# Kernel tuning notes

Measured on AMD Instinct MI355X. Metric: run time of the kernel, lower is better.

## Reference

```python
import jax, jax.numpy as jnp
import numpy as np

TOPK = 60            # candidates kept by top-k
THRESHOLD = 0.15     # score threshold (post-sigmoid)
NMS_THRESHOLD = 0.05 # IoU overlap for suppression/matching
NMS_TOPK = 20        # max kept detections per image
CROP_SIZE = (96, 96, 96)
AVG_TOPN = 7         # max matched boxes averaged per kept box


def setup_inputs() -> dict:
    key = jax.random.key(0)
    k1, k2, k3 = jax.random.split(key, 3)
    B, D, H, W = 256, 24, 24, 24
    Cls = jax.random.normal(k1, (B, 1, D, H, W), dtype=jnp.float32)
    # sizes in [1,7) voxels so 3D boxes at stride-4 anchor spacing overlap
    Shape = jax.random.uniform(k2, (B, 3, D, H, W), dtype=jnp.float32) * 6.0 + 1.0
    Offset = jax.random.normal(k3, (B, 3, D, H, W), dtype=jnp.float32)
    return {"Cls": Cls, "Shape": Shape, "Offset": Offset}


def _decode(Cls, Shape, Offset):
    # make_anchors + bbox_decode: centers = (anchor + offset) * stride, sizes = Shape
    B, _, D, H, W = Cls.shape
    stride = jnp.float32(CROP_SIZE[0] / D)  # 96/24 = 4
    gz, gy, gx = jnp.meshgrid(jnp.arange(D, dtype=jnp.float32),
                              jnp.arange(H, dtype=jnp.float32),
                              jnp.arange(W, dtype=jnp.float32), indexing="ij")
    anchors = jnp.stack([gz, gy, gx], -1).reshape(-1, 3)            # [N,3]
    scores = jax.nn.sigmoid(Cls.reshape(B, -1))                     # [B,N] (is_logits=True)
    shapes = Shape.reshape(B, 3, -1).transpose(0, 2, 1)             # [B,N,3]
    offsets = Offset.reshape(B, 3, -1).transpose(0, 2, 1)           # [B,N,3]
    centers = (anchors[None] + offsets) * stride
    bboxes = jnp.concatenate([centers, shapes], -1)                 # [B,N,6] = (z,y,x,d,h,w)
    return scores, bboxes


def _iou_matrix(det):
    # axis-aligned 3D IoU between all pairs of the TOPK candidate boxes
    c, s = det[:, 2:5], det[:, 5:8]
    lo, hi = c - 0.5 * s, c + 0.5 * s
    inter = jnp.prod(jnp.maximum(jnp.minimum(hi[:, None], hi[None]) -
                                 jnp.maximum(lo[:, None], lo[None]), 0.0), -1)
    vol = jnp.prod(s, -1)
    return inter / (vol[:, None] + vol[None] - inter)


def _nms_image(scores, bboxes):
    # top-k (sorted descending, as torch.topk) then masked iterative NMS with
    # IoU-matched top-7 box averaging, emitting a fixed [NMS_TOPK, 8] table.
    topk_s, topk_i = jax.lax.top_k(scores, TOPK)
    valid = topk_s > THRESHOLD
    det = jnp.concatenate([jnp.ones((TOPK, 1), jnp.float32),
                           topk_s[:, None], bboxes[topk_i]], -1)    # [TOPK,8]
    iou = _iou_matrix(det)
    ar = jnp.arange(TOPK)

    def step(suppressed, _):
        avail = valid & ~suppressed
        any_avail = jnp.any(avail)
        idx = jnp.argmax(avail)  # first available = highest remaining score
        matched = avail & ((iou[idx] > NMS_THRESHOLD) | (ar == idx))
        rank = jnp.cumsum(matched) - 1            # matched are already score-sorted
        sel = matched & (rank < AVG_TOPN)
        top_n = jnp.minimum(jnp.sum(matched), AVG_TOPN)
        avg = jnp.sum(det * sel[:, None].astype(det.dtype), 0) / jnp.maximum(top_n, 1).astype(det.dtype)
        avg = avg.at[0].set(1.0).at[1].set(det[idx, 1])  # flag=1, prob = best score
        row = jnp.where(top_n > 1, avg, det[idx])
        row = jnp.where(any_avail, row, -jnp.ones(8, det.dtype))
        suppressed = jnp.where(any_avail, suppressed | matched, suppressed)
        return suppressed, row

    _, rows = jax.lax.scan(step, jnp.zeros(TOPK, dtype=bool), None, length=NMS_TOPK)
    return rows  # [NMS_TOPK, 8]


def reference(Cls, Shape, Offset):
    scores, bboxes = _decode(Cls, Shape, Offset)
    return jax.vmap(_nms_image)(scores, bboxes)  # [B, NMS_TOPK, 8]
```

## Files before the change

kernel.cpp:

```cpp
#include <hip/hip_runtime.h>
#include <math.h>

#define N_ANCH 13824
#define TPB 1024
#define K_TOP 60
#define K_NMS 20
#define AVG_TOPN 7
#define CAP 2048
#define PIVOT_KEY 0xC0100000u

__device__ __forceinline__ unsigned mono_key(float x) {
  unsigned m = __float_as_uint(x);
  return (m & 0x80000000u) ? ~m : (m | 0x80000000u);
}

__global__ __launch_bounds__(TPB)
void detpp_kernel(const float* __restrict__ Cls,
                  const float* __restrict__ Shp,
                  const float* __restrict__ Off,
                  float* __restrict__ Out) {
  __shared__ __align__(16) unsigned long long list[CAP];
  __shared__ float det[K_TOP][9];
  __shared__ unsigned long long Mrow[K_TOP];
  __shared__ unsigned int cnt2;

  const int b = blockIdx.x;
  const int t = threadIdx.x;
  const int lane = t & 63;
  const size_t cbase = (size_t)b * N_ANCH;

  if (t == 0) cnt2 = 0;
  if (t < K_TOP) Mrow[t] = 1ull << t;

  const float4* C4 = (const float4*)(Cls + cbase);
  float4 v0 = C4[t];
  float4 v1 = C4[1024 + t];
  float4 v2 = C4[2048 + t];
  const bool tail = (t < 384);
  float4 v3 = tail ? C4[3072 + t] : make_float4(0.f, 0.f, 0.f, 0.f);
  __syncthreads();

  unsigned k[16];
  k[0]  = mono_key(v0.x); k[1]  = mono_key(v0.y); k[2]  = mono_key(v0.z); k[3]  = mono_key(v0.w);
  k[4]  = mono_key(v1.x); k[5]  = mono_key(v1.y); k[6]  = mono_key(v1.z); k[7]  = mono_key(v1.w);
  k[8]  = mono_key(v2.x); k[9]  = mono_key(v2.y); k[10] = mono_key(v2.z); k[11] = mono_key(v2.w);
  if (tail) {
    k[12] = mono_key(v3.x); k[13] = mono_key(v3.y); k[14] = mono_key(v3.z); k[15] = mono_key(v3.w);
  } else {
    k[12] = 0u; k[13] = 0u; k[14] = 0u; k[15] = 0u;
  }

  int cnt = 0;
  #pragma unroll
  for (int q = 0; q < 16; ++q) cnt += (k[q] > PIVOT_KEY) ? 1 : 0;

  int pfx = cnt;
  #pragma unroll
  for (int d = 1; d < 64; d <<= 1) {
    int o = __shfl_up(pfx, d, 64);
    if (lane >= d) pfx += o;
  }
  const int excl = pfx - cnt;
  int wtot = __shfl(pfx, 63, 64);
  unsigned wbase = 0;
  if (lane == 63) wbase = atomicAdd(&cnt2, (unsigned)wtot);
  wbase = (unsigned)__shfl((int)wbase, 63, 64);

  {
    int off = (int)wbase + excl;
    #pragma unroll
    for (int q = 0; q < 16; ++q) {
      if (k[q] > PIVOT_KEY) {
        int base_i = (q < 4) ? (t << 2) : (q < 8) ? ((1024 + t) << 2)
                     : (q < 12) ? ((2048 + t) << 2) : ((3072 + t) << 2);
        int i = base_i + (q & 3);
        if (off < CAP)
          list[off] = ((unsigned long long)k[q] << 32) | (unsigned)(~i);
        off++;
      }
    }
  }
  __syncthreads();

  const unsigned total = cnt2;
  const bool fast = (total >= (unsigned)K_TOP) && (total <= (unsigned)CAP);

  if (fast) {
    const int tot = (int)total;
    unsigned long long e = 0ull;
    int i = 0;
    float o0 = 0.f, o1 = 0.f, o2 = 0.f, s0 = 0.f, s1 = 0.f, s2 = 0.f;
    if (t < tot) {
      e = list[t];
      i = (int)(~(unsigned)(e & 0xffffffffull));
      size_t bb = (size_t)b * 3 * N_ANCH + (size_t)i;
      o0 = Off[bb]; o1 = Off[bb + N_ANCH]; o2 = Off[bb + 2 * N_ANCH];
      s0 = Shp[bb]; s1 = Shp[bb + N_ANCH]; s2 = Shp[bb + 2 * N_ANCH];
    }
    if (t < tot) {
      int r = 0;
      const ulonglong2* L2 = (const ulonglong2*)list;
      const int half = tot >> 1;
      for (int j2 = 0; j2 < half; ++j2) {
        ulonglong2 p = L2[j2];
        r += (p.x > e) ? 1 : 0;
        r += (p.y > e) ? 1 : 0;
      }
      if (tot & 1) r += (list[tot - 1] > e) ? 1 : 0;
      if (r < K_TOP) {
        unsigned m = (unsigned)(e >> 32);
        unsigned bits = (m & 0x80000000u) ? (m & 0x7fffffffu) : ~m;
        float lg = __uint_as_float(bits);
        int iz = i / 576;
        int r2 = i - iz * 576;
        int iy = r2 / 24;
        int ix = r2 - iy * 24;
        det[r][0] = 1.0f;
        det[r][1] = 1.0f / (1.0f + expf(-lg));
        det[r][2] = ((float)iz + o0) * 4.0f;
        det[r][3] = ((float)iy + o1) * 4.0f;
        det[r][4] = ((float)ix + o2) * 4.0f;
        det[r][5] = s0;
        det[r][6] = s1;
        det[r][7] = s2;
      }
    }
  } else {
    for (int i = t; i < N_ANCH; i += TPB) {
      unsigned ki = mono_key(Cls[cbase + i]);
      unsigned long long e = ((unsigned long long)ki << 32) | (unsigned)(~i);
      int r = 0;
      for (int j = 0; j < N_ANCH; ++j) {
        unsigned kj = mono_key(Cls[cbase + j]);
        unsigned long long ej = ((unsigned long long)kj << 32) | (unsigned)(~j);
        r += (ej > e) ? 1 : 0;
      }
      if (r < K_TOP) {
        unsigned m = (unsigned)(e >> 32);
        unsigned bits = (m & 0x80000000u) ? (m & 0x7fffffffu) : ~m;
        float lg = __uint_as_float(bits);
        int iz = i / 576;
        int r2 = i - iz * 576;
        int iy = r2 / 24;
        int ix = r2 - iy * 24;
        size_t bb = (size_t)b * 3 * N_ANCH + (size_t)i;
        det[r][0] = 1.0f;
        det[r][1] = 1.0f / (1.0f + expf(-lg));
        det[r][2] = ((float)iz + Off[bb]) * 4.0f;
        det[r][3] = ((float)iy + Off[bb + N_ANCH]) * 4.0f;
        det[r][4] = ((float)ix + Off[bb + 2 * N_ANCH]) * 4.0f;
        det[r][5] = Shp[bb];
        det[r][6] = Shp[bb + N_ANCH];
        det[r][7] = Shp[bb + 2 * N_ANCH];
      }
    }
  }
  __syncthreads();

  for (int p = t; p < 1800; p += TPB) {
    int ii = p / 30;
    int kk = p - ii * 30;
    int jj = ii + 1 + kk; if (jj >= 60) jj -= 60;
    float cz1 = det[ii][2], cy1 = det[ii][3], cx1 = det[ii][4];
    float sz1 = det[ii][5], sy1 = det[ii][6], sx1 = det[ii][7];
    float cz2 = det[jj][2], cy2 = det[jj][3], cx2 = det[jj][4];
    float sz2 = det[jj][5], sy2 = det[jj][6], sx2 = det[jj][7];
    float lz1 = cz1 - 0.5f * sz1, hz1 = cz1 + 0.5f * sz1;
    float ly1 = cy1 - 0.5f * sy1, hy1 = cy1 + 0.5f * sy1;
    float lx1 = cx1 - 0.5f * sx1, hx1 = cx1 + 0.5f * sx1;
    float lz2 = cz2 - 0.5f * sz2, hz2 = cz2 + 0.5f * sz2;
    float ly2 = cy2 - 0.5f * sy2, hy2 = cy2 + 0.5f * sy2;
    float lx2 = cx2 - 0.5f * sx2, hx2 = cx2 + 0.5f * sx2;
    float dz = fmaxf(fminf(hz1, hz2) - fmaxf(lz1, lz2), 0.0f);
    float dy = fmaxf(fminf(hy1, hy2) - fmaxf(ly1, ly2), 0.0f);
    float dx = fmaxf(fminf(hx1, hx2) - fmaxf(lx1, lx2), 0.0f);
    float inter = (dz * dy) * dx;
    float v1 = (sz1 * sy1) * sx1;
    float v2 = (sz2 * sy2) * sx2;
    float iouv = inter / (v1 + v2 - inter);
    if (iouv > 0.05f) {
      atomicOr(&Mrow[ii], 1ull << jj);
      atomicOr(&Mrow[jj], 1ull << ii);
    }
  }
  __syncthreads();

  const int w = t >> 6;
  if (w < 3) {
    const bool in = (lane < K_TOP);
    float myscore = in ? det[lane][1] : 0.0f;
    unsigned long long M = in ? Mrow[lane] : 0ull;
    unsigned long long validm = __ballot(in && (myscore > 0.15f));
    unsigned long long suppressed = 0ull;
    float* outb = Out + (size_t)b * K_NMS * 8;

    const int my_s = (w << 3) + (lane >> 3);
    const int c = lane & 7;
    const bool active = (my_s < K_NMS);
    unsigned long long my_matched = 0ull;
    int my_idx = 0;
    bool my_any = false;

    #pragma unroll
    for (int step = 0; step < K_NMS; ++step) {
      unsigned long long avail = validm & ~suppressed;
      const bool any = (avail != 0ull);
      int idx = any ? (int)__builtin_ctzll(avail) : 0;
      unsigned mlo = (unsigned)__builtin_amdgcn_readlane((int)(unsigned)(M & 0xffffffffull), idx);
      unsigned mhi = (unsigned)__builtin_amdgcn_readlane((int)(unsigned)(M >> 32), idx);
      unsigned long long matched = any ? (avail & (((unsigned long long)mhi << 32) | mlo)) : 0ull;
      if (step == my_s) { my_matched = matched; my_idx = idx; my_any = any; }
      suppressed |= matched;
    }

    if (active) {
      int cm = __popcll(my_matched);
      int top_n = cm < AVG_TOPN ? cm : AVG_TOPN;
      float sum = 0.0f;
      unsigned long long mm = my_matched;
      #pragma unroll
      for (int q = 0; q < AVG_TOPN; ++q) {
        int bq = mm ? (int)__builtin_ctzll(mm) : 0;
        if (q < top_n) sum += det[bq][c];
        mm &= mm - 1ull;
      }
      float r = sum / (float)(top_n > 0 ? top_n : 1);
      if (c == 0) r = 1.0f;
      if (c == 1) r = det[my_idx][1];
      if (!my_any) r = -1.0f;
      outb[my_s * 8 + c] = r;
    }
  }
}

extern "C" void kernel_launch(void* const* d_in, const int* in_sizes, int n_in,
                              void* d_out, int out_size, void* d_ws, size_t ws_size,
                              hipStream_t stream) {
  const float* Cls = (const float*)d_in[0];
  const float* Shp = (const float*)d_in[1];
  const float* Off = (const float*)d_in[2];
  float* Out = (float*)d_out;
  int B = in_sizes[0] / N_ANCH;
  detpp_kernel<<<B, TPB, 0, stream>>>(Cls, Shp, Off, Out);
}
```

Baseline: 112.8 us.

## Split fused kernel into prune and NMS kernels via global workspace

```diff
diff --git a/kernel.cpp b/kernel.cpp
--- a/kernel.cpp
+++ b/kernel.cpp
@@ -2,11 +2,10 @@
 #include <math.h>
 
 #define N_ANCH 13824
-#define TPB 1024
 #define K_TOP 60
 #define K_NMS 20
 #define AVG_TOPN 7
-#define CAP 2048
+#define CAP_G 511
 #define PIVOT_KEY 0xC0100000u
 
 __device__ __forceinline__ unsigned mono_key(float x) {
@@ -14,24 +13,15 @@
   return (m & 0x80000000u) ? ~m : (m | 0x80000000u);
 }
 
-__global__ __launch_bounds__(TPB)
-void detpp_kernel(const float* __restrict__ Cls,
-                  const float* __restrict__ Shp,
-                  const float* __restrict__ Off,
-                  float* __restrict__ Out) {
-  __shared__ __align__(16) unsigned long long list[CAP];
-  __shared__ float det[K_TOP][9];
-  __shared__ unsigned long long Mrow[K_TOP];
+__global__ __launch_bounds__(1024)
+void prune_kernel(const float* __restrict__ Cls, unsigned long long* __restrict__ W) {
   __shared__ unsigned int cnt2;
-
   const int b = blockIdx.x;
   const int t = threadIdx.x;
   const int lane = t & 63;
   const size_t cbase = (size_t)b * N_ANCH;
 
   if (t == 0) cnt2 = 0;
-  if (t < K_TOP) Mrow[t] = 1ull << t;
-
   const float4* C4 = (const float4*)(Cls + cbase);
   float4 v0 = C4[t];
   float4 v1 = C4[1024 + t];
@@ -66,6 +56,7 @@
   if (lane == 63) wbase = atomicAdd(&cnt2, (unsigned)wtot);
   wbase = (unsigned)__shfl((int)wbase, 63, 64);
 
+  unsigned long long* Wb = W + (size_t)b * (CAP_G + 1);
   {
     int off = (int)wbase + excl;
     #pragma unroll
@@ -74,30 +65,48 @@
         int base_i = (q < 4) ? (t << 2) : (q < 8) ? ((1024 + t) << 2)
                      : (q < 12) ? ((2048 + t) << 2) : ((3072 + t) << 2);
         int i = base_i + (q & 3);
-        if (off < CAP)
-          list[off] = ((unsigned long long)k[q] << 32) | (unsigned)(~i);
+        if (off < CAP_G)
+          Wb[1 + off] = ((unsigned long long)k[q] << 32) | (unsigned)(~i);
         off++;
       }
     }
   }
   __syncthreads();
-
-  const unsigned total = cnt2;
-  const bool fast = (total >= (unsigned)K_TOP) && (total <= (unsigned)CAP);
+  if (t == 0) Wb[0] = (unsigned long long)cnt2;
+}
+
+__global__ __launch_bounds__(256)
+void nms_kernel(const float* __restrict__ Cls,
+                const float* __restrict__ Shp,
+                const float* __restrict__ Off,
+                const unsigned long long* __restrict__ W,
+                float* __restrict__ Out) {
+  __shared__ __align__(16) unsigned long long list[CAP_G + 1];
+  __shared__ float det[K_TOP][9];
+  __shared__ unsigned long long Mrow[K_TOP];
+
+  const int b = blockIdx.x;
+  const int t = threadIdx.x;
+  const int lane = t & 63;
+  const size_t cbase = (size_t)b * N_ANCH;
+  const unsigned long long* Wb = W + (size_t)b * (CAP_G + 1);
+
+  if (t < K_TOP) Mrow[t] = 1ull << t;
+
+  const int tot = (int)(unsigned)Wb[0];
+  const bool fast = (tot >= K_TOP) && (tot <= CAP_G);
+  const int stot = fast ? tot : 0;
+  if (t < stot) list[t] = Wb[1 + t];
+  if (t + 256 < stot) list[t + 256] = Wb[1 + t + 256];
+  __syncthreads();
 
   if (fast) {
-    const int tot = (int)total;
-    unsigned long long e = 0ull;
-    int i = 0;
-    float o0 = 0.f, o1 = 0.f, o2 = 0.f, s0 = 0.f, s1 = 0.f, s2 = 0.f;
-    if (t < tot) {
-      e = list[t];
-      i = (int)(~(unsigned)(e & 0xffffffffull));
+    for (int s = t; s < tot; s += 256) {
+      const unsigned long long e = list[s];
+      const int i = (int)(~(unsigned)(e & 0xffffffffull));
       size_t bb = (size_t)b * 3 * N_ANCH + (size_t)i;
-      o0 = Off[bb]; o1 = Off[bb + N_ANCH]; o2 = Off[bb + 2 * N_ANCH];
-      s0 = Shp[bb]; s1 = Shp[bb + N_ANCH]; s2 = Shp[bb + 2 * N_ANCH];
-    }
-    if (t < tot) {
+      float o0 = Off[bb], o1 = Off[bb + N_ANCH], o2 = Off[bb + 2 * N_ANCH];
+      float s0 = Shp[bb], s1 = Shp[bb + N_ANCH], s2 = Shp[bb + 2 * N_ANCH];
       int r = 0;
       const ulonglong2* L2 = (const ulonglong2*)list;
       const int half = tot >> 1;
@@ -126,7 +135,7 @@
       }
     }
   } else {
-    for (int i = t; i < N_ANCH; i += TPB) {
+    for (int i = t; i < N_ANCH; i += 256) {
       unsigned ki = mono_key(Cls[cbase + i]);
       unsigned long long e = ((unsigned long long)ki << 32) | (unsigned)(~i);
       int r = 0;
@@ -157,7 +166,7 @@
   }
   __syncthreads();
 
-  for (int p = t; p < 1800; p += TPB) {
+  for (int p = t; p < 1800; p += 256) {
     int ii = p / 30;
     int kk = p - ii * 30;
     int jj = ii + 1 + kk; if (jj >= 60) jj -= 60;
@@ -240,6 +249,8 @@
   const float* Shp = (const float*)d_in[1];
   const float* Off = (const float*)d_in[2];
   float* Out = (float*)d_out;
+  unsigned long long* W = (unsigned long long*)d_ws;
   int B = in_sizes[0] / N_ANCH;
-  detpp_kernel<<<B, TPB, 0, stream>>>(Cls, Shp, Off, Out);
-}
+  prune_kernel<<<B, 1024, 0, stream>>>(Cls, W);
+  nms_kernel<<<B, 256, 0, stream>>>(Cls, Shp, Off, W, Out);
+}
```

After: 117.8 us. 4.5% more time.

## Replace atomics with per-wave count scan and ballot-built IoU mask rows

Applied to the files above, without the earlier changes.

```diff
diff --git a/kernel.cpp b/kernel.cpp
--- a/kernel.cpp
+++ b/kernel.cpp
@@ -22,15 +22,13 @@
   __shared__ __align__(16) unsigned long long list[CAP];
   __shared__ float det[K_TOP][9];
   __shared__ unsigned long long Mrow[K_TOP];
-  __shared__ unsigned int cnt2;
+  __shared__ unsigned int wcounts[16];
 
   const int b = blockIdx.x;
   const int t = threadIdx.x;
   const int lane = t & 63;
+  const int w = t >> 6;
   const size_t cbase = (size_t)b * N_ANCH;
-
-  if (t == 0) cnt2 = 0;
-  if (t < K_TOP) Mrow[t] = 1ull << t;
 
   const float4* C4 = (const float4*)(Cls + cbase);
   float4 v0 = C4[t];
@@ -38,7 +36,6 @@
   float4 v2 = C4[2048 + t];
   const bool tail = (t < 384);
   float4 v3 = tail ? C4[3072 + t] : make_float4(0.f, 0.f, 0.f, 0.f);
-  __syncthreads();
 
   unsigned k[16];
   k[0]  = mono_key(v0.x); k[1]  = mono_key(v0.y); k[2]  = mono_key(v0.z); k[3]  = mono_key(v0.w);
@@ -61,10 +58,16 @@
     if (lane >= d) pfx += o;
   }
   const int excl = pfx - cnt;
-  int wtot = __shfl(pfx, 63, 64);
-  unsigned wbase = 0;
-  if (lane == 63) wbase = atomicAdd(&cnt2, (unsigned)wtot);
-  wbase = (unsigned)__shfl((int)wbase, 63, 64);
+  if (lane == 63) wcounts[w] = (unsigned)pfx;
+  __syncthreads();
+
+  unsigned wbase = 0, total = 0;
+  #pragma unroll
+  for (int w2 = 0; w2 < 16; ++w2) {
+    unsigned c = wcounts[w2];
+    if (w2 < w) wbase += c;
+    total += c;
+  }
 
   {
     int off = (int)wbase + excl;
@@ -82,22 +85,16 @@
   }
   __syncthreads();
 
-  const unsigned total = cnt2;
   const bool fast = (total >= (unsigned)K_TOP) && (total <= (unsigned)CAP);
 
   if (fast) {
     const int tot = (int)total;
-    unsigned long long e = 0ull;
-    int i = 0;
-    float o0 = 0.f, o1 = 0.f, o2 = 0.f, s0 = 0.f, s1 = 0.f, s2 = 0.f;
-    if (t < tot) {
-      e = list[t];
-      i = (int)(~(unsigned)(e & 0xffffffffull));
+    for (int s = t; s < tot; s += TPB) {
+      const unsigned long long e = list[s];
+      const int i = (int)(~(unsigned)(e & 0xffffffffull));
       size_t bb = (size_t)b * 3 * N_ANCH + (size_t)i;
-      o0 = Off[bb]; o1 = Off[bb + N_ANCH]; o2 = Off[bb + 2 * N_ANCH];
-      s0 = Shp[bb]; s1 = Shp[bb + N_ANCH]; s2 = Shp[bb + 2 * N_ANCH];
-    }
-    if (t < tot) {
+      float o0 = Off[bb], o1 = Off[bb + N_ANCH], o2 = Off[bb + 2 * N_ANCH];
+      float s0 = Shp[bb], s1 = Shp[bb + N_ANCH], s2 = Shp[bb + 2 * N_ANCH];
       int r = 0;
       const ulonglong2* L2 = (const ulonglong2*)list;
       const int half = tot >> 1;
@@ -157,14 +154,15 @@
   }
   __syncthreads();
 
-  for (int p = t; p < 1800; p += TPB) {
-    int ii = p / 30;
-    int kk = p - ii * 30;
-    int jj = ii + 1 + kk; if (jj >= 60) jj -= 60;
-    float cz1 = det[ii][2], cy1 = det[ii][3], cx1 = det[ii][4];
-    float sz1 = det[ii][5], sy1 = det[ii][6], sx1 = det[ii][7];
-    float cz2 = det[jj][2], cy2 = det[jj][3], cx2 = det[jj][4];
-    float sz2 = det[jj][5], sy2 = det[jj][6], sx2 = det[jj][7];
+  #pragma unroll
+  for (int it = 0; it < 4; ++it) {
+    const int ii = (w << 2) + it;
+    bool m = false;
+    if (ii < K_TOP && lane < K_TOP) {
+      float cz1 = det[ii][2], cy1 = det[ii][3], cx1 = det[ii][4];
+      float sz1 = det[ii][5], sy1 = det[ii][6], sx1 = det[ii][7];
+      float cz2 = det[lane][2], cy2 = det[lane][3], cx2 = det[lane][4];
+      float sz2 = det[lane][5], sy2 = det[lane][6], sx2 = det[lane][7];
     float lz1 = cz1 - 0.5f * sz1, hz1 = cz1 + 0.5f * sz1;
     float ly1 = cy1 - 0.5f * sy1, hy1 = cy1 + 0.5f * sy1;
     float lx1 = cx1 - 0.5f * sx1, hx1 = cx1 + 0.5f * sx1;
@@ -178,14 +176,13 @@
     float v1 = (sz1 * sy1) * sx1;
     float v2 = (sz2 * sy2) * sx2;
     float iouv = inter / (v1 + v2 - inter);
-    if (iouv > 0.05f) {
-      atomicOr(&Mrow[ii], 1ull << jj);
-      atomicOr(&Mrow[jj], 1ull << ii);
-    }
-  }
-  __syncthreads();
-
-  const int w = t >> 6;
+      m = (iouv > 0.05f) || (lane == ii);
+    }
+    unsigned long long bal = __ballot(m);
+    if (ii < K_TOP && lane == 0) Mrow[ii] = bal;
+  }
+  __syncthreads();
+
   if (w < 3) {
     const bool in = (lane < K_TOP);
     float myscore = in ? det[lane][1] : 0.0f;
```

Measured after the change: 115.2 us. 2.2% more time.
